# Kernel optimization log

Hardware: AMD Instinct MI355X
Metric: run time of the kernel (lower is better)

Reference implementation:

```python
import jax, jax.numpy as jnp
import numpy as np

STRIDE, PAD, DIL, KH, KW = 1, 1, 1, 3, 3


def _bilinear_gather(img, y, xq):
    # img: (Cin,H,W); y,xq: (K,Ho,Wo) float sample coords. Zero padding outside.
    H, W = img.shape[1], img.shape[2]
    y0 = jnp.floor(y); x0 = jnp.floor(xq)
    wy1 = y - y0; wx1 = xq - x0
    wy0 = 1.0 - wy1; wx0 = 1.0 - wx1

    def g(yi, xi):
        valid = (yi >= 0) & (yi <= H - 1) & (xi >= 0) & (xi <= W - 1)
        yc = jnp.clip(yi, 0, H - 1).astype(jnp.int32)
        xc = jnp.clip(xi, 0, W - 1).astype(jnp.int32)
        v = img[:, yc, xc]  # (Cin,K,Ho,Wo)
        return jnp.where(valid[None], v, 0.0)

    return ((wy0 * wx0)[None] * g(y0, x0) + (wy0 * wx1)[None] * g(y0, x0 + 1)
            + (wy1 * wx0)[None] * g(y0 + 1, x0) + (wy1 * wx1)[None] * g(y0 + 1, x0 + 1))


def _deform_conv2d(x, offset, weight, bias):
    B, Cin, H, W = x.shape
    Cout = weight.shape[0]
    Ho, Wo = offset.shape[2], offset.shape[3]
    K = KH * KW
    off = offset.reshape(B, K, 2, Ho, Wo)  # (y,x) pairs per kernel tap, row-major
    ki, kj = jnp.meshgrid(jnp.arange(KH), jnp.arange(KW), indexing='ij')
    base_y = (jnp.arange(Ho) * STRIDE - PAD)[None, :, None] + (ki.reshape(K) * DIL)[:, None, None]  # (K,Ho,1)
    base_x = (jnp.arange(Wo) * STRIDE - PAD)[None, None, :] + (kj.reshape(K) * DIL)[:, None, None]  # (K,1,Wo)
    ys = base_y.astype(x.dtype) + off[:, :, 0]  # (B,K,Ho,Wo)
    xs = base_x.astype(x.dtype) + off[:, :, 1]
    samples = jax.vmap(_bilinear_gather)(x, ys, xs)  # (B,Cin,K,Ho,Wo)
    out = jnp.einsum('bckhw,ock->bohw', samples, weight.reshape(Cout, Cin, K))
    return out + bias[None, :, None, None]


def setup_inputs() -> dict:
    key = jax.random.key(0)
    k1, k2, k3, k4, k5 = jax.random.split(key, 5)
    x = jax.random.normal(k1, (8, 64, 96, 96), dtype=jnp.float32)
    offset = jax.random.normal(k2, (8, 18, 96, 96), dtype=jnp.float32)
    x2 = jax.random.normal(k3, (8, 64, 96, 96), dtype=jnp.float32)
    weight = jax.random.normal(k4, (64, 64, 3, 3), dtype=jnp.float32) * 0.04  # ~kaiming scale for fan_in=576
    bias = jax.random.normal(k5, (64,), dtype=jnp.float32) * 0.1
    return {'x': x, 'offset': offset, 'x2': x2, 'weight': weight, 'bias': bias}


def reference(x, offset, x2, weight, bias):
    out = _deform_conv2d(x, offset, weight, bias)
    out = out + x2
    return jnp.clip(out, 0.0, 6.0)  # ReLU6
```

## Files before the change

kernel.cpp:

```cpp
#include <hip/hip_runtime.h>
#include <math.h>

#define B_    8
#define CIN   64
#define COUT  64
#define H_    96
#define W_    96
#define HW    9216
#define KK    9
#define PIX   64
#define NTHR  256
#define BLKS_PER_B 144
#define SP    72

typedef __attribute__((ext_vector_type(8))) short short8;
typedef __attribute__((ext_vector_type(4))) float floatx4;

#if __has_builtin(__builtin_amdgcn_fdot2_f32_bf16)
#define HAVE_DOT2 1
typedef __attribute__((ext_vector_type(2))) __bf16 bf16x2;
static __device__ __forceinline__ bf16x2 as_bf16x2(unsigned u) {
    union { unsigned u; bf16x2 v; } c; c.u = u; return c.v;
}
#else
#define HAVE_DOT2 0
#endif

static __device__ __forceinline__ unsigned short f2bf(float f) {
    unsigned u = __float_as_uint(f);
    unsigned r = (u + 0x7FFFu + ((u >> 16) & 1u)) >> 16;
    return (unsigned short)r;
}
static __device__ __forceinline__ float bf_lo(unsigned u) { return __uint_as_float(u << 16); }
static __device__ __forceinline__ float bf_hi(unsigned u) { return __uint_as_float(u & 0xFFFF0000u); }

static __device__ __forceinline__ unsigned pack_bf2(float vl, float vh) {
    unsigned rl = __float_as_uint(vl) + 0x8000u;
    unsigned rh = __float_as_uint(vh) + 0x8000u;
    return __builtin_amdgcn_perm(rh, rl, 0x07060302u);
}

__global__ __launch_bounds__(256) void prep_kernel(const float* __restrict__ x,
                                                   const float* __restrict__ w,
                                                   unsigned int* __restrict__ xTu,
                                                   unsigned short* __restrict__ wA) {
    __shared__ float tile[64][65];
    if (blockIdx.x < B_ * BLKS_PER_B) {
        int b   = blockIdx.x / BLKS_PER_B;
        int hw0 = (blockIdx.x % BLKS_PER_B) * 64;
        int lane = threadIdx.x & 63;
        int r    = threadIdx.x >> 6;
        const float* xb = x + (size_t)b * CIN * HW;
        #pragma unroll
        for (int i = 0; i < 16; ++i) {
            int c = r + i * 4;
            tile[c][lane] = xb[(size_t)c * HW + hw0 + lane];
        }
        __syncthreads();
        unsigned int* dst = xTu + ((size_t)b * HW + hw0) * 32;
        int c2 = threadIdx.x & 31;
        int pr = threadIdx.x >> 5;
        #pragma unroll
        for (int i = 0; i < 8; ++i) {
            int p = pr + i * 8;
            unsigned pk = (unsigned)f2bf(tile[2 * c2][p]) |
                          ((unsigned)f2bf(tile[2 * c2 + 1][p]) << 16);
            dst[(size_t)p * 32 + c2] = pk;
        }
    } else {
        int gid  = (blockIdx.x - B_ * BLKS_PER_B) * 256 + threadIdx.x;
        int lane = gid & 63;
        int mt   = (gid >> 6) & 3;
        int kap  = gid >> 8;
        int o    = mt * 16 + (lane & 15);
        int cb   = (kap & 1) * 32 + (lane >> 4) * 8;
        int tap  = kap >> 1;
        short8 v;
        #pragma unroll
        for (int j = 0; j < 8; ++j)
            v[j] = (short)f2bf(w[o * 576 + (cb + j) * 9 + tap]);
        *(short8*)&wA[(size_t)gid * 8] = v;
    }
}

static __device__ __forceinline__ void issue_tap_loads(
    const unsigned int* __restrict__ xb, const ushort4* eoS,
    int t, int wq, int half, int c2, unsigned (&u)[8][4])
{
    #pragma unroll
    for (int j = 0; j < 8; ++j) {
        int p = wq * 16 + j * 2 + half;
        ushort4 o4 = eoS[t * 64 + p];
        u[j][0] = xb[((size_t)o4.x << 5) + c2];
        u[j][1] = xb[((size_t)o4.y << 5) + c2];
        u[j][2] = xb[((size_t)o4.z << 5) + c2];
        u[j][3] = xb[((size_t)o4.w << 5) + c2];
    }
}

#if HAVE_DOT2
static __device__ __forceinline__ void compute_tap(
    const uint2* awP, short* Sbuf, int t, int wq, int half, int c2,
    const unsigned (&u)[8][4])
{
    unsigned int* Su = (unsigned int*)Sbuf;
    #pragma unroll
    for (int j = 0; j < 8; ++j) {
        int p = wq * 16 + j * 2 + half;
        uint2 aw = awP[t * 64 + p];
        unsigned lo01 = __builtin_amdgcn_perm(u[j][1], u[j][0], 0x05040100u);
        unsigned hi01 = __builtin_amdgcn_perm(u[j][1], u[j][0], 0x07060302u);
        unsigned lo23 = __builtin_amdgcn_perm(u[j][3], u[j][2], 0x05040100u);
        unsigned hi23 = __builtin_amdgcn_perm(u[j][3], u[j][2], 0x07060302u);
        float vl = __builtin_amdgcn_fdot2_f32_bf16(as_bf16x2(lo01), as_bf16x2(aw.x), 0.0f, false);
        vl = __builtin_amdgcn_fdot2_f32_bf16(as_bf16x2(lo23), as_bf16x2(aw.y), vl, false);
        float vh = __builtin_amdgcn_fdot2_f32_bf16(as_bf16x2(hi01), as_bf16x2(aw.x), 0.0f, false);
        vh = __builtin_amdgcn_fdot2_f32_bf16(as_bf16x2(hi23), as_bf16x2(aw.y), vh, false);
        Su[p * (SP / 2) + c2] = pack_bf2(vl, vh);
    }
}
#else
static __device__ __forceinline__ void compute_tap(
    const float4* ewP, short* Sbuf, int t, int wq, int half, int c2,
    const unsigned (&u)[8][4])
{
    unsigned int* Su = (unsigned int*)Sbuf;
    #pragma unroll
    for (int j = 0; j < 8; ++j) {
        int p = wq * 16 + j * 2 + half;
        float4 w4 = ewP[t * 64 + p];
        float vl = w4.x * bf_lo(u[j][0]);
        vl = fmaf(w4.y, bf_lo(u[j][1]), vl);
        vl = fmaf(w4.z, bf_lo(u[j][2]), vl);
        vl = fmaf(w4.w, bf_lo(u[j][3]), vl);
        float vh = w4.x * bf_hi(u[j][0]);
        vh = fmaf(w4.y, bf_hi(u[j][1]), vh);
        vh = fmaf(w4.z, bf_hi(u[j][2]), vh);
        vh = fmaf(w4.w, bf_hi(u[j][3]), vh);
        Su[p * (SP / 2) + c2] = pack_bf2(vl, vh);
    }
}
#endif

__global__ __launch_bounds__(256, 3) void deform_mfma_kernel(
    const unsigned int* __restrict__ xTu, const float* __restrict__ offset,
    const float* __restrict__ x2, const float* __restrict__ bias,
    const unsigned short* __restrict__ wA, float* __restrict__ out)
{
#if HAVE_DOT2
    __shared__ uint2   awP[KK * PIX];
#else
    __shared__ float4  awP[KK * PIX];
#endif
    __shared__ ushort4 eoS[KK * PIX];
    __shared__ __align__(16) short S[PIX * SP];

    const int tid  = threadIdx.x;
    const int b    = blockIdx.x & 7;
    const int pix0 = (blockIdx.x >> 3) * PIX;
    const int lane = tid & 63;
    const int wq   = __builtin_amdgcn_readfirstlane(tid >> 6);

    const unsigned int* xb = xTu + (size_t)b * HW * 32;
    const float* offb = offset + (size_t)b * (18 * HW);
    const short8* wAv = (const short8*)wA;

    for (int el = lane; el < KK * 16; el += 64) {
        int t  = el >> 4;
        int p  = (wq << 4) + (el & 15);
        int e  = t * 64 + p;
        int hw = pix0 + p;
        int h  = hw / W_;
        int w  = hw - h * W_;
        float offy = offb[(size_t)(2 * t) * HW + hw];
        float offx = offb[(size_t)(2 * t + 1) * HW + hw];
        int ki = t / 3;
        int kj = t - ki * 3;
        float yy = (float)(h - 1 + ki) + offy;
        float xx = (float)(w - 1 + kj) + offx;
        float y0f = floorf(yy), x0f = floorf(xx);
        float wy1 = yy - y0f, wx1 = xx - x0f;
        float wy0 = 1.0f - wy1, wx0 = 1.0f - wx1;
        int y0 = (int)y0f, x0 = (int)x0f;
        int y1 = y0 + 1, x1 = x0 + 1;
        float ay0 = (y0 >= 0 && y0 < H_) ? wy0 : 0.0f;
        float ay1 = (y1 >= 0 && y1 < H_) ? wy1 : 0.0f;
        float ax0 = (x0 >= 0 && x0 < W_) ? wx0 : 0.0f;
        float ax1 = (x1 >= 0 && x1 < W_) ? wx1 : 0.0f;
        float w00 = ay0 * ax0, w01 = ay0 * ax1, w10 = ay1 * ax0, w11 = ay1 * ax1;
        int y0c = min(max(y0, 0), H_ - 1), y1c = min(max(y1, 0), H_ - 1);
        int x0c = min(max(x0, 0), W_ - 1), x1c = min(max(x1, 0), W_ - 1);
#if HAVE_DOT2
        awP[e] = make_uint2((unsigned)f2bf(w00) | ((unsigned)f2bf(w01) << 16),
                            (unsigned)f2bf(w10) | ((unsigned)f2bf(w11) << 16));
#else
        awP[e] = make_float4(w00, w01, w10, w11);
#endif
        eoS[e] = make_ushort4((unsigned short)(y0c * W_ + x0c),
                              (unsigned short)(y0c * W_ + x1c),
                              (unsigned short)(y1c * W_ + x0c),
                              (unsigned short)(y1c * W_ + x1c));
    }

    floatx4 acc[4];
    #pragma unroll
    for (int mt = 0; mt < 4; ++mt) acc[mt] = (floatx4){0.f, 0.f, 0.f, 0.f};

    const int c2   = lane & 31;
    const int half = lane >> 5;
    const int n_   = lane & 15;
    const int qk   = (lane >> 4) * 8;
    const int prow = wq * 16 + n_;

    unsigned u[2][8][4];
    issue_tap_loads(xb, eoS, 0, wq, half, c2, u[0]);

    #pragma unroll
    for (int t = 0; t < KK; ++t) {
        const int buf = t & 1;

        if (t < KK - 1)
            issue_tap_loads(xb, eoS, t + 1, wq, half, c2, u[(t + 1) & 1]);

        short8 aA0[4], aA1[4];
        #pragma unroll
        for (int mt = 0; mt < 4; ++mt) {
            aA0[mt] = wAv[(size_t)((t * 2    ) * 4 + mt) * 64 + lane];
            aA1[mt] = wAv[(size_t)((t * 2 + 1) * 4 + mt) * 64 + lane];
        }

        compute_tap(awP, S, t, wq, half, c2, u[buf]);

        short8 b0 = *(const short8*)&S[prow * SP + qk];
        short8 b1 = *(const short8*)&S[prow * SP + 32 + qk];
        #pragma unroll
        for (int mt = 0; mt < 4; ++mt) {
            acc[mt] = __builtin_amdgcn_mfma_f32_16x16x32_bf16(aA0[mt], b0, acc[mt], 0, 0, 0);
            acc[mt] = __builtin_amdgcn_mfma_f32_16x16x32_bf16(aA1[mt], b1, acc[mt], 0, 0, 0);
        }
    }

    {
        const int quad4 = (lane >> 4) * 4;
        const size_t hwcol = (size_t)pix0 + wq * 16 + n_;
        #pragma unroll
        for (int mt = 0; mt < 4; ++mt) {
            #pragma unroll
            for (int reg = 0; reg < 4; ++reg) {
                int oc = mt * 16 + quad4 + reg;
                size_t idx = ((size_t)(b * COUT + oc)) * HW + hwcol;
                float r = acc[mt][reg] + bias[oc] + x2[idx];
                r = fminf(fmaxf(r, 0.0f), 6.0f);
                out[idx] = r;
            }
        }
    }
}

__global__ __launch_bounds__(256, 4) void deform_nchw_kernel(
    const float* __restrict__ x, const float* __restrict__ offset,
    const float* __restrict__ x2, const float* __restrict__ weight,
    const float* __restrict__ bias, float* __restrict__ out)
{
    __shared__ float sT[CIN * PIX];
    __shared__ float ewS[4][KK * PIX];
    __shared__ int   eoS[4][KK * PIX];

    const int tid  = threadIdx.x;
    const int b    = blockIdx.x / BLKS_PER_B;
    const int pix0 = (blockIdx.x % BLKS_PER_B) * PIX;
    const int lane = tid & 63;
    const int wq   = __builtin_amdgcn_readfirstlane(tid >> 6);

    const float* xb   = x + (size_t)b * (CIN * HW);
    const float* offb = offset + (size_t)b * (18 * HW);

    for (int e = tid; e < KK * PIX; e += NTHR) {
        int k  = e >> 6;
        int p  = e & 63;
        int hw = pix0 + p;
        int h  = hw / W_;
        int w  = hw - h * W_;
        float offy = offb[(size_t)(2 * k) * HW + hw];
        float offx = offb[(size_t)(2 * k + 1) * HW + hw];
        int ki = k / 3;
        int kj = k - ki * 3;
        float yy = (float)(h - 1 + ki) + offy;
        float xx = (float)(w - 1 + kj) + offx;
        float y0f = floorf(yy), x0f = floorf(xx);
        float wy1 = yy - y0f, wx1 = xx - x0f;
        float wy0 = 1.0f - wy1, wx0 = 1.0f - wx1;
        int y0 = (int)y0f, x0 = (int)x0f;
        int y1 = y0 + 1, x1 = x0 + 1;
        float vy0 = (y0 >= 0 && y0 < H_) ? 1.0f : 0.0f;
        float vy1 = (y1 >= 0 && y1 < H_) ? 1.0f : 0.0f;
        float vx0 = (x0 >= 0 && x0 < W_) ? 1.0f : 0.0f;
        float vx1 = (x1 >= 0 && x1 < W_) ? 1.0f : 0.0f;
        int y0c = min(max(y0, 0), H_ - 1), y1c = min(max(y1, 0), H_ - 1);
        int x0c = min(max(x0, 0), W_ - 1), x1c = min(max(x1, 0), W_ - 1);
        ewS[0][e] = wy0 * wx0 * vy0 * vx0;
        ewS[1][e] = wy0 * wx1 * vy0 * vx1;
        ewS[2][e] = wy1 * wx0 * vy1 * vx0;
        ewS[3][e] = wy1 * wx1 * vy1 * vx1;
        eoS[0][e] = y0c * W_ + x0c;
        eoS[1][e] = y0c * W_ + x1c;
        eoS[2][e] = y1c * W_ + x0c;
        eoS[3][e] = y1c * W_ + x1c;
    }

    float acc[16];
    #pragma unroll
    for (int i = 0; i < 16; ++i) acc[i] = 0.0f;

    __syncthreads();

    for (int k = 0; k < KK; ++k) {
        {
            const int eb = k * 64 + lane;
            const float w0 = ewS[0][eb], w1 = ewS[1][eb], w2 = ewS[2][eb], w3 = ewS[3][eb];
            const int   o0 = eoS[0][eb], o1 = eoS[1][eb], o2 = eoS[2][eb], o3 = eoS[3][eb];
            const int cg = tid >> 6;
            const float* xc = xb + (size_t)(cg * 16) * HW;
            #pragma unroll
            for (int i = 0; i < 16; ++i) {
                float v = w0 * xc[o0] + w1 * xc[o1] + w2 * xc[o2] + w3 * xc[o3];
                sT[(cg * 16 + i) * 64 + lane] = v;
                xc += HW;
            }
        }
        __syncthreads();
        {
            #pragma unroll 2
            for (int c = 0; c < 64; ++c) {
                float sv = sT[c * 64 + lane];
                #pragma unroll
                for (int oi = 0; oi < 16; ++oi)
                    acc[oi] = fmaf(weight[(wq * 16 + oi) * 576 + c * 9 + k], sv, acc[oi]);
            }
        }
        __syncthreads();
    }

    const size_t obase = ((size_t)b * COUT + wq * 16) * HW + pix0 + lane;
    #pragma unroll
    for (int oi = 0; oi < 16; ++oi) {
        float r = acc[oi] + bias[wq * 16 + oi] + x2[obase + (size_t)oi * HW];
        r = fminf(fmaxf(r, 0.0f), 6.0f);
        out[obase + (size_t)oi * HW] = r;
    }
}

extern "C" void kernel_launch(void* const* d_in, const int* in_sizes, int n_in,
                              void* d_out, int out_size, void* d_ws, size_t ws_size,
                              hipStream_t stream) {
    const float* x      = (const float*)d_in[0];
    const float* offset = (const float*)d_in[1];
    const float* x2     = (const float*)d_in[2];
    const float* weight = (const float*)d_in[3];
    const float* bias   = (const float*)d_in[4];
    float* out          = (float*)d_out;

    const int grid = B_ * BLKS_PER_B;

    const size_t xT_bytes = (size_t)B_ * HW * CIN * sizeof(unsigned short);
    const size_t wA_bytes = (size_t)18 * 4 * 64 * 8 * sizeof(unsigned short);

    if (ws_size >= xT_bytes + wA_bytes) {
        unsigned int*   xTu = (unsigned int*)d_ws;
        unsigned short* wA  = (unsigned short*)((char*)d_ws + xT_bytes);
        prep_kernel<<<grid + 18, 256, 0, stream>>>(x, weight, xTu, wA);
        deform_mfma_kernel<<<grid, NTHR, 0, stream>>>(xTu, offset, x2, bias, wA, out);
    } else {
        deform_nchw_kernel<<<grid, NTHR, 0, stream>>>(x, offset, x2, weight, bias, out);
    }
}
```

Before: 121.8 us.

## Apply bilinear weights after MFMA per corner instead of interpolating into LDS

Rather than interpolating the four bilinear corners into a bf16 LDS staging buffer and running one MFMA per tap, each corner's gathered bf16 channel vector is loaded straight into MFMA B registers. Four MFMA products are computed per tap and scaled by the per-pixel bilinear weight in fp32. This drops the LDS staging buffer, its writes and reads, the dot2 interpolation, and one bf16 rounding of the interpolated values. In exchange it does four times the MFMA work plus 16 extra FMAs per tap per tile, and gives up the explicit double-buffered prefetch of the gathers.

```diff
diff --git a/kernel.cpp b/kernel.cpp
--- a/kernel.cpp
+++ b/kernel.cpp
@@ -11,33 +11,14 @@
 #define PIX   64
 #define NTHR  256
 #define BLKS_PER_B 144
-#define SP    72
 
 typedef __attribute__((ext_vector_type(8))) short short8;
 typedef __attribute__((ext_vector_type(4))) float floatx4;
-
-#if __has_builtin(__builtin_amdgcn_fdot2_f32_bf16)
-#define HAVE_DOT2 1
-typedef __attribute__((ext_vector_type(2))) __bf16 bf16x2;
-static __device__ __forceinline__ bf16x2 as_bf16x2(unsigned u) {
-    union { unsigned u; bf16x2 v; } c; c.u = u; return c.v;
-}
-#else
-#define HAVE_DOT2 0
-#endif
 
 static __device__ __forceinline__ unsigned short f2bf(float f) {
     unsigned u = __float_as_uint(f);
     unsigned r = (u + 0x7FFFu + ((u >> 16) & 1u)) >> 16;
     return (unsigned short)r;
-}
-static __device__ __forceinline__ float bf_lo(unsigned u) { return __uint_as_float(u << 16); }
-static __device__ __forceinline__ float bf_hi(unsigned u) { return __uint_as_float(u & 0xFFFF0000u); }
-
-static __device__ __forceinline__ unsigned pack_bf2(float vl, float vh) {
-    unsigned rl = __float_as_uint(vl) + 0x8000u;
-    unsigned rh = __float_as_uint(vh) + 0x8000u;
-    return __builtin_amdgcn_perm(rh, rl, 0x07060302u);
 }
 
 __global__ __launch_bounds__(256) void prep_kernel(const float* __restrict__ x,
@@ -83,77 +64,13 @@
     }
 }
 
-static __device__ __forceinline__ void issue_tap_loads(
-    const unsigned int* __restrict__ xb, const ushort4* eoS,
-    int t, int wq, int half, int c2, unsigned (&u)[8][4])
-{
-    #pragma unroll
-    for (int j = 0; j < 8; ++j) {
-        int p = wq * 16 + j * 2 + half;
-        ushort4 o4 = eoS[t * 64 + p];
-        u[j][0] = xb[((size_t)o4.x << 5) + c2];
-        u[j][1] = xb[((size_t)o4.y << 5) + c2];
-        u[j][2] = xb[((size_t)o4.z << 5) + c2];
-        u[j][3] = xb[((size_t)o4.w << 5) + c2];
-    }
-}
-
-#if HAVE_DOT2
-static __device__ __forceinline__ void compute_tap(
-    const uint2* awP, short* Sbuf, int t, int wq, int half, int c2,
-    const unsigned (&u)[8][4])
-{
-    unsigned int* Su = (unsigned int*)Sbuf;
-    #pragma unroll
-    for (int j = 0; j < 8; ++j) {
-        int p = wq * 16 + j * 2 + half;
-        uint2 aw = awP[t * 64 + p];
-        unsigned lo01 = __builtin_amdgcn_perm(u[j][1], u[j][0], 0x05040100u);
-        unsigned hi01 = __builtin_amdgcn_perm(u[j][1], u[j][0], 0x07060302u);
-        unsigned lo23 = __builtin_amdgcn_perm(u[j][3], u[j][2], 0x05040100u);
-        unsigned hi23 = __builtin_amdgcn_perm(u[j][3], u[j][2], 0x07060302u);
-        float vl = __builtin_amdgcn_fdot2_f32_bf16(as_bf16x2(lo01), as_bf16x2(aw.x), 0.0f, false);
-        vl = __builtin_amdgcn_fdot2_f32_bf16(as_bf16x2(lo23), as_bf16x2(aw.y), vl, false);
-        float vh = __builtin_amdgcn_fdot2_f32_bf16(as_bf16x2(hi01), as_bf16x2(aw.x), 0.0f, false);
-        vh = __builtin_amdgcn_fdot2_f32_bf16(as_bf16x2(hi23), as_bf16x2(aw.y), vh, false);
-        Su[p * (SP / 2) + c2] = pack_bf2(vl, vh);
-    }
-}
-#else
-static __device__ __forceinline__ void compute_tap(
-    const float4* ewP, short* Sbuf, int t, int wq, int half, int c2,
-    const unsigned (&u)[8][4])
-{
-    unsigned int* Su = (unsigned int*)Sbuf;
-    #pragma unroll
-    for (int j = 0; j < 8; ++j) {
-        int p = wq * 16 + j * 2 + half;
-        float4 w4 = ewP[t * 64 + p];
-        float vl = w4.x * bf_lo(u[j][0]);
-        vl = fmaf(w4.y, bf_lo(u[j][1]), vl);
-        vl = fmaf(w4.z, bf_lo(u[j][2]), vl);
-        vl = fmaf(w4.w, bf_lo(u[j][3]), vl);
-        float vh = w4.x * bf_hi(u[j][0]);
-        vh = fmaf(w4.y, bf_hi(u[j][1]), vh);
-        vh = fmaf(w4.z, bf_hi(u[j][2]), vh);
-        vh = fmaf(w4.w, bf_hi(u[j][3]), vh);
-        Su[p * (SP / 2) + c2] = pack_bf2(vl, vh);
-    }
-}
-#endif
-
 __global__ __launch_bounds__(256, 3) void deform_mfma_kernel(
     const unsigned int* __restrict__ xTu, const float* __restrict__ offset,
     const float* __restrict__ x2, const float* __restrict__ bias,
     const unsigned short* __restrict__ wA, float* __restrict__ out)
 {
-#if HAVE_DOT2
-    __shared__ uint2   awP[KK * PIX];
-#else
     __shared__ float4  awP[KK * PIX];
-#endif
     __shared__ ushort4 eoS[KK * PIX];
-    __shared__ __align__(16) short S[PIX * SP];
 
     const int tid  = threadIdx.x;
     const int b    = blockIdx.x & 7;
@@ -161,9 +78,9 @@
     const int lane = tid & 63;
     const int wq   = __builtin_amdgcn_readfirstlane(tid >> 6);
 
-    const unsigned int* xb = xTu + (size_t)b * HW * 32;
     const float* offb = offset + (size_t)b * (18 * HW);
     const short8* wAv = (const short8*)wA;
+    const char*  xbB  = (const char*)xTu + (size_t)b * HW * 128;
 
     for (int el = lane; el < KK * 16; el += 64) {
         int t  = el >> 4;
@@ -187,15 +104,9 @@
         float ay1 = (y1 >= 0 && y1 < H_) ? wy1 : 0.0f;
         float ax0 = (x0 >= 0 && x0 < W_) ? wx0 : 0.0f;
         float ax1 = (x1 >= 0 && x1 < W_) ? wx1 : 0.0f;
-        float w00 = ay0 * ax0, w01 = ay0 * ax1, w10 = ay1 * ax0, w11 = ay1 * ax1;
         int y0c = min(max(y0, 0), H_ - 1), y1c = min(max(y1, 0), H_ - 1);
         int x0c = min(max(x0, 0), W_ - 1), x1c = min(max(x1, 0), W_ - 1);
-#if HAVE_DOT2
-        awP[e] = make_uint2((unsigned)f2bf(w00) | ((unsigned)f2bf(w01) << 16),
-                            (unsigned)f2bf(w10) | ((unsigned)f2bf(w11) << 16));
-#else
-        awP[e] = make_float4(w00, w01, w10, w11);
-#endif
+        awP[e] = make_float4(ay0 * ax0, ay0 * ax1, ay1 * ax0, ay1 * ax1);
         eoS[e] = make_ushort4((unsigned short)(y0c * W_ + x0c),
                               (unsigned short)(y0c * W_ + x1c),
                               (unsigned short)(y1c * W_ + x0c),
@@ -205,23 +116,14 @@
     floatx4 acc[4];
     #pragma unroll
     for (int mt = 0; mt < 4; ++mt) acc[mt] = (floatx4){0.f, 0.f, 0.f, 0.f};
-
-    const int c2   = lane & 31;
-    const int half = lane >> 5;
-    const int n_   = lane & 15;
-    const int qk   = (lane >> 4) * 8;
-    const int prow = wq * 16 + n_;
-
-    unsigned u[2][8][4];
-    issue_tap_loads(xb, eoS, 0, wq, half, c2, u[0]);
+    const floatx4 zero4 = (floatx4){0.f, 0.f, 0.f, 0.f};
+
+    const int n_  = lane & 15;
+    const int h16 = (lane >> 4) * 16;
+    const int pxl = wq * 16 + n_;
 
     #pragma unroll
     for (int t = 0; t < KK; ++t) {
-        const int buf = t & 1;
-
-        if (t < KK - 1)
-            issue_tap_loads(xb, eoS, t + 1, wq, half, c2, u[(t + 1) & 1]);
-
         short8 aA0[4], aA1[4];
         #pragma unroll
         for (int mt = 0; mt < 4; ++mt) {
@@ -229,14 +131,30 @@
             aA1[mt] = wAv[(size_t)((t * 2 + 1) * 4 + mt) * 64 + lane];
         }
 
-        compute_tap(awP, S, t, wq, half, c2, u[buf]);
-
-        short8 b0 = *(const short8*)&S[prow * SP + qk];
-        short8 b1 = *(const short8*)&S[prow * SP + 32 + qk];
-        #pragma unroll
-        for (int mt = 0; mt < 4; ++mt) {
-            acc[mt] = __builtin_amdgcn_mfma_f32_16x16x32_bf16(aA0[mt], b0, acc[mt], 0, 0, 0);
-            acc[mt] = __builtin_amdgcn_mfma_f32_16x16x32_bf16(aA1[mt], b1, acc[mt], 0, 0, 0);
+        ushort4 o4 = eoS[t * 64 + pxl];
+        float4  w4 = awP[t * 64 + pxl];
+        const int   oq[4] = {o4.x, o4.y, o4.z, o4.w};
+        const float wc[4] = {w4.x, w4.y, w4.z, w4.w};
+
+        short8 Blo[4], Bhi[4];
+        #pragma unroll
+        for (int q = 0; q < 4; ++q) {
+            const char* base = xbB + (size_t)oq[q] * 128 + h16;
+            Blo[q] = *(const short8*)(base);
+            Bhi[q] = *(const short8*)(base + 64);
+        }
+
+        #pragma unroll
+        for (int q = 0; q < 4; ++q) {
+            #pragma unroll
+            for (int mt = 0; mt < 4; ++mt) {
+                floatx4 d = __builtin_amdgcn_mfma_f32_16x16x32_bf16(aA0[mt], Blo[q], zero4, 0, 0, 0);
+                d = __builtin_amdgcn_mfma_f32_16x16x32_bf16(aA1[mt], Bhi[q], d, 0, 0, 0);
+                acc[mt][0] = fmaf(wc[q], d[0], acc[mt][0]);
+                acc[mt][1] = fmaf(wc[q], d[1], acc[mt][1]);
+                acc[mt][2] = fmaf(wc[q], d[2], acc[mt][2]);
+                acc[mt][3] = fmaf(wc[q], d[3], acc[mt][3]);
+            }
         }
     }
 
```

New measurement: 144.1 us. 1.18x slower.
